# Kernel tuning notes

Hardware: AMD Instinct MI355X
Metric: run time of the kernel (lower is better)

Reference implementation:

```python
import jax, jax.numpy as jnp
import numpy as np

EPS = 1e-09

def setup_inputs() -> dict:
    key = jax.random.key(0)
    k1, k2, k3 = jax.random.split(key, 3)
    B, C, H, W = 16, 512, 64, 64
    K = 64  # node_num
    x = jax.random.normal(k1, (B, C, H, W), dtype=jnp.float32)
    anchor = jax.random.uniform(k2, (K, C), dtype=jnp.float32)
    sigma_raw = jax.random.uniform(k3, (K, C), dtype=jnp.float32)
    return {"x": x, "anchor": anchor, "sigma_raw": sigma_raw}

def _l2norm(v, axis):
    return v / jnp.maximum(jnp.linalg.norm(v, axis=axis, keepdims=True), 1e-12)

def reference(x, anchor, sigma_raw):
    B, C, H, W = x.shape
    K = anchor.shape[0]
    N = H * W
    sigma = jax.nn.sigmoid(sigma_raw)               # [K, C]
    xf = x.reshape(B, C, N).transpose(0, 2, 1)      # [B, N, C] descriptors

    # squared Mahalanobis-like distance ||(x - a_k)/s_k||^2 via expansion
    # (avoids materializing the [B, N, K, C] residual the torch loop builds)
    inv_s2 = 1.0 / (sigma * sigma)                  # [K, C]
    a_s2 = anchor * inv_s2                          # [K, C]
    const = jnp.sum(anchor * a_s2, axis=1)          # [K]
    d2 = (jnp.einsum('bnc,kc->bnk', xf * xf, inv_s2)
          - 2.0 * jnp.einsum('bnc,kc->bnk', xf, a_s2)
          + const[None, None, :])                   # [B, N, K]
    logits = (-0.5 * d2).transpose(0, 2, 1)         # [B, K, N]
    soft_assign = jax.nn.softmax(logits, axis=1)    # softmax over nodes

    # aggregation: nodes[b,k,c] = sum_n w * (x - a_k)/s_k / (sum_n w + eps)
    w_sum = jnp.sum(soft_assign, axis=2)            # [B, K]
    wx = jnp.einsum('bkn,bnc->bkc', soft_assign, xf)  # [B, K, C]
    nodes = (wx - w_sum[:, :, None] * anchor[None]) / sigma[None]
    nodes = nodes / (w_sum[:, :, None] + EPS)       # [B, K, C]

    nodes = _l2norm(nodes, axis=2)                  # intra-normalize per node
    flat = _l2norm(nodes.reshape(B, -1), axis=1)    # global L2
    # faithful to torch: flat [B, K*C] reinterpreted (no transpose) as [B, C, K]
    return flat.reshape(B, C, K), soft_assign
```

## Files before the change

kernel.cpp:

```cpp
#include <hip/hip_runtime.h>
#include <math.h>

#define B_ 16
#define C_ 512
#define N_ 4096
#define K_ 64

#define OFF_PBIG    0
#define OFF_CONST   131072
#define OFF_INVSIG  131136
#define OFF_WSUM    163904
#define OFF_GSUM    164928
#define OFF_WXP     165120

typedef short bf16x8 __attribute__((ext_vector_type(8)));
typedef float f32x16 __attribute__((ext_vector_type(16)));

union U4 { uint4 u; bf16x8 b; };

__device__ __forceinline__ unsigned hi16(float f) { return __float_as_uint(f) >> 16; }
__device__ __forceinline__ float fromhi(unsigned h) { return __uint_as_float(h << 16); }
__device__ __forceinline__ unsigned pk(float lo, float hi) {
  return (__float_as_uint(lo) >> 16) | (__float_as_uint(hi) & 0xFFFF0000u);
}

__global__ void k_prep(const float* __restrict__ anchor,
                       const float* __restrict__ sraw,
                       unsigned* __restrict__ pbig,
                       float* __restrict__ constk,
                       float* __restrict__ invsig,
                       float* __restrict__ wsum,
                       float* __restrict__ gsum) {
  const int k = blockIdx.x;
  const int t = threadIdx.x;
  __shared__ float s_is2[C_], s_m[C_];
  __shared__ float red[4];
  float part = 0.f;
#pragma unroll
  for (int r = 0; r < 2; r++) {
    int c = r * 256 + t;
    float a = anchor[k * C_ + c];
    float sg = 1.f / (1.f + __expf(-sraw[k * C_ + c]));
    float is = 1.f / sg;
    float is2 = is * is;
    s_is2[c] = is2;
    s_m[c] = -2.f * a * is2;
    invsig[k * C_ + c] = is;
    part = fmaf(a * a, is2, part);
  }
  float v = part;
#pragma unroll
  for (int off = 32; off; off >>= 1) v += __shfl_down(v, off);
  if ((t & 63) == 0) red[t >> 6] = v;
  __syncthreads();
  if (t == 0) constk[k] = red[0] + red[1] + red[2] + red[3];
#pragma unroll
  for (int r = 0; r < 2; r++) {
    int c = r * 256 + t;
    float is2 = s_is2[c], m = s_m[c];
    unsigned ih = hi16(is2);
    unsigned il = hi16(is2 - fromhi(ih));
    unsigned mh = hi16(m);
    unsigned ml = hi16(m - fromhi(mh));
    unsigned* p = pbig + (size_t)k * 2048 + c * 4;
    p[0] = ih | (il << 16);
    p[1] = ih | (mh << 16);
    p[2] = ml | (mh << 16);
    p[3] = 0u;
  }
  if (k == 0) {
    for (int i = t; i < B_ * K_; i += 256) wsum[i] = 0.f;
    if (t < B_) gsum[t] = 0.f;
  }
}

__global__ __launch_bounds__(256) void k_dist(
    const float* __restrict__ x,
    const unsigned* __restrict__ pbig,
    const float* __restrict__ constk,
    float* __restrict__ soft,
    float* __restrict__ wsum) {
  const int b = blockIdx.y;
  const int tid = threadIdx.x;
  const int wid = tid >> 6, lane = tid & 63, l31 = lane & 31, lh = lane >> 5;
  const int n0 = blockIdx.x * 128 + wid * 32;
  __shared__ unsigned ldsA[64 * 132];
  __shared__ float csh[64];
  if (tid < 64) csh[tid] = constk[tid];

  f32x16 acc[2];
#pragma unroll
  for (int kt = 0; kt < 2; kt++)
#pragma unroll
    for (int i = 0; i < 16; i++) acc[kt][i] = 0.f;

  const float* xb = x + (size_t)b * (C_ * N_);
  const uint4* src = (const uint4*)pbig;

  uint4 preg[8];
#pragma unroll
  for (int it = 0; it < 8; it++) {
    int flat = tid + it * 256;
    preg[it] = src[(size_t)(flat >> 5) * 512 + (flat & 31)];
  }
  float xcur[16], xnext[16];
#pragma unroll
  for (int i = 0; i < 16; i++)
    xcur[i] = xb[(size_t)(i * 2 + lh) * N_ + n0 + l31];

  for (int chunk = 0; chunk < 16; chunk++) {
#pragma unroll
    for (int it = 0; it < 8; it++) {
      int flat = tid + it * 256;
      *(uint4*)&ldsA[(flat >> 5) * 132 + (flat & 31) * 4] = preg[it];
    }
    __syncthreads();
    if (chunk < 15) {
#pragma unroll
      for (int it = 0; it < 8; it++) {
        int flat = tid + it * 256;
        preg[it] = src[(size_t)(flat >> 5) * 512 + (chunk + 1) * 32 + (flat & 31)];
      }
#pragma unroll
      for (int i = 0; i < 16; i++)
        xnext[i] = xb[(size_t)((chunk + 1) * 32 + i * 2 + lh) * N_ + n0 + l31];
    }
#pragma unroll
    for (int kstep = 0; kstep < 16; kstep++) {
      U4 a0, a1;
      a0.u = *(const uint4*)&ldsA[l31 * 132 + kstep * 8 + lh * 4];
      a1.u = *(const uint4*)&ldsA[(32 + l31) * 132 + kstep * 8 + lh * 4];
      float xv = xcur[kstep];
      float x2 = xv * xv;
      unsigned u = __float_as_uint(xv);
      unsigned u2 = __float_as_uint(x2);
      unsigned uhf = u & 0xFFFF0000u;
      unsigned u2hf = u2 & 0xFFFF0000u;
      float xl = xv - __uint_as_float(uhf);
      float x2l = x2 - __uint_as_float(u2hf);
      U4 bf;
      bf.u.x = (u2 >> 16) | u2hf;
      bf.u.y = (__float_as_uint(x2l) >> 16) | uhf;
      bf.u.z = (u >> 16) | (__float_as_uint(xl) & 0xFFFF0000u);
      bf.u.w = 0u;
      acc[0] = __builtin_amdgcn_mfma_f32_32x32x16_bf16(a0.b, bf.b, acc[0], 0, 0, 0);
      acc[1] = __builtin_amdgcn_mfma_f32_32x32x16_bf16(a1.b, bf.b, acc[1], 0, 0, 0);
    }
    __syncthreads();
#pragma unroll
    for (int i = 0; i < 16; i++) xcur[i] = xnext[i];
  }

  float mm = -3.4e38f;
#pragma unroll
  for (int kt = 0; kt < 2; kt++)
#pragma unroll
    for (int r = 0; r < 16; r++) {
      int k = kt * 32 + (r & 3) + 8 * (r >> 2) + 4 * lh;
      float l = -0.5f * (acc[kt][r] + csh[k]);
      acc[kt][r] = l;
      mm = fmaxf(mm, l);
    }
  mm = fmaxf(mm, __shfl_xor(mm, 32));
  float ss = 0.f;
#pragma unroll
  for (int kt = 0; kt < 2; kt++)
#pragma unroll
    for (int r = 0; r < 16; r++) {
      float e = __expf(acc[kt][r] - mm);
      acc[kt][r] = e;
      ss += e;
    }
  ss += __shfl_xor(ss, 32);
  float inv = 1.f / ss;

  float* softb = soft + (size_t)b * (K_ * N_);
#pragma unroll
  for (int kt = 0; kt < 2; kt++)
#pragma unroll
    for (int r = 0; r < 16; r++) {
      float w = acc[kt][r] * inv;
      acc[kt][r] = w;
      int k = kt * 32 + (r & 3) + 8 * (r >> 2) + 4 * lh;
      softb[(size_t)k * N_ + n0 + l31] = w;
    }
#pragma unroll
  for (int kt = 0; kt < 2; kt++)
#pragma unroll
    for (int r = 0; r < 16; r++) {
      float v = acc[kt][r];
      v += __shfl_xor(v, 1);
      v += __shfl_xor(v, 2);
      v += __shfl_xor(v, 4);
      v += __shfl_xor(v, 8);
      v += __shfl_xor(v, 16);
      if (l31 == 0) {
        int k = kt * 32 + (r & 3) + 8 * (r >> 2) + 4 * lh;
        atomicAdd(&wsum[b * K_ + k], v);
      }
    }
}

__global__ __launch_bounds__(256) void k_agg(const float* __restrict__ x,
                                             const float* __restrict__ soft,
                                             float* __restrict__ wxp) {
  const int ct = blockIdx.x;
  const int nt = blockIdx.y;
  const int b = blockIdx.z;
  const int tid = threadIdx.x;
  const int wid = tid >> 6, lane = tid & 63, l31 = lane & 31, lh = lane >> 5;
  __shared__ unsigned sA[64 * 36];
  __shared__ unsigned sX[128 * 36];

  f32x16 acc[2];
#pragma unroll
  for (int kt = 0; kt < 2; kt++)
#pragma unroll
    for (int i = 0; i < 16; i++) acc[kt][i] = 0.f;

  const float* sb = soft + (size_t)b * (K_ * N_) + nt * 1024;
  const float* xg = x + ((size_t)b * C_ + ct * 128) * N_ + nt * 1024;
  const int srow = tid >> 2, scol = (tid & 3) * 16;
  const int xrow = tid >> 1, xcol = (tid & 1) * 32;

  float4 sreg[4], xreg[8];
#pragma unroll
  for (int q = 0; q < 4; q++)
    sreg[q] = *(const float4*)&sb[(size_t)srow * N_ + scol + q * 4];
#pragma unroll
  for (int q = 0; q < 8; q++)
    xreg[q] = *(const float4*)&xg[(size_t)xrow * N_ + xcol + q * 4];

  for (int ch = 0; ch < 16; ch++) {
    {
      uint4 w0 = make_uint4(pk(sreg[0].x, sreg[0].y), pk(sreg[0].z, sreg[0].w),
                            pk(sreg[1].x, sreg[1].y), pk(sreg[1].z, sreg[1].w));
      uint4 w1 = make_uint4(pk(sreg[2].x, sreg[2].y), pk(sreg[2].z, sreg[2].w),
                            pk(sreg[3].x, sreg[3].y), pk(sreg[3].z, sreg[3].w));
      *(uint4*)&sA[srow * 36 + (tid & 3) * 8] = w0;
      *(uint4*)&sA[srow * 36 + (tid & 3) * 8 + 4] = w1;
#pragma unroll
      for (int h = 0; h < 4; h++) {
        uint4 v = make_uint4(
            pk(xreg[h * 2].x, xreg[h * 2].y), pk(xreg[h * 2].z, xreg[h * 2].w),
            pk(xreg[h * 2 + 1].x, xreg[h * 2 + 1].y),
            pk(xreg[h * 2 + 1].z, xreg[h * 2 + 1].w));
        *(uint4*)&sX[xrow * 36 + (tid & 1) * 16 + h * 4] = v;
      }
    }
    __syncthreads();
    if (ch < 15) {
      int base = (ch + 1) * 64;
#pragma unroll
      for (int q = 0; q < 4; q++)
        sreg[q] = *(const float4*)&sb[(size_t)srow * N_ + base + scol + q * 4];
#pragma unroll
      for (int q = 0; q < 8; q++)
        xreg[q] = *(const float4*)&xg[(size_t)xrow * N_ + base + xcol + q * 4];
    }
#pragma unroll
    for (int kk = 0; kk < 4; kk++) {
      U4 a0, a1, bf;
      a0.u = *(const uint4*)&sA[l31 * 36 + kk * 8 + lh * 4];
      a1.u = *(const uint4*)&sA[(32 + l31) * 36 + kk * 8 + lh * 4];
      bf.u = *(const uint4*)&sX[(wid * 32 + l31) * 36 + kk * 8 + lh * 4];
      acc[0] = __builtin_amdgcn_mfma_f32_32x32x16_bf16(a0.b, bf.b, acc[0], 0, 0, 0);
      acc[1] = __builtin_amdgcn_mfma_f32_32x32x16_bf16(a1.b, bf.b, acc[1], 0, 0, 0);
    }
    __syncthreads();
  }
  float* outp = wxp + (((size_t)nt * B_ + b) * K_) * C_ + ct * 128 + wid * 32 + l31;
#pragma unroll
  for (int kt = 0; kt < 2; kt++)
#pragma unroll
    for (int r = 0; r < 16; r++) {
      int k = kt * 32 + (r & 3) + 8 * (r >> 2) + 4 * lh;
      outp[(size_t)k * C_] = acc[kt][r];
    }
}

__global__ void k_nodes(const float* __restrict__ wxp,
                        const float* __restrict__ wsum,
                        const float* __restrict__ anchor,
                        const float* __restrict__ invsig,
                        float* __restrict__ out0,
                        float* __restrict__ gsum) {
  const int k = blockIdx.x, b = blockIdx.y;
  const int tid = threadIdx.x;
  float wsv = wsum[b * K_ + k];
  float winv = 1.f / (wsv + 1e-9f);
  float vals[4];
  float local = 0.f;
#pragma unroll
  for (int r = 0; r < 4; r++) {
    int c = r * 128 + tid;
    float w = 0.f;
#pragma unroll
    for (int p = 0; p < 4; p++)
      w += wxp[(((size_t)p * B_ + b) * K_ + k) * C_ + c];
    float v = (w - wsv * anchor[k * C_ + c]) * invsig[k * C_ + c] * winv;
    vals[r] = v;
    local = fmaf(v, v, local);
  }
  float v = local;
#pragma unroll
  for (int off = 32; off; off >>= 1) v += __shfl_down(v, off);
  __shared__ float red[2];
  if ((tid & 63) == 0) red[tid >> 6] = v;
  __syncthreads();
  float sumsq = red[0] + red[1];
  float norm = sqrtf(sumsq);
  float scale = 1.f / fmaxf(norm, 1e-12f);
#pragma unroll
  for (int r = 0; r < 4; r++) {
    int c = r * 128 + tid;
    out0[((size_t)b * K_ + k) * C_ + c] = vals[r] * scale;
  }
  if (tid == 0) atomicAdd(&gsum[b], sumsq * scale * scale);
}

__global__ void k_final(float* __restrict__ out0,
                        const float* __restrict__ gsum) {
  for (int i = blockIdx.x * 256 + threadIdx.x; i < B_ * K_ * C_;
       i += gridDim.x * 256) {
    int b = i >> 15;
    out0[i] = out0[i] * (1.f / fmaxf(sqrtf(gsum[b]), 1e-12f));
  }
}

extern "C" void kernel_launch(void* const* d_in, const int* in_sizes, int n_in,
                              void* d_out, int out_size, void* d_ws, size_t ws_size,
                              hipStream_t stream) {
  const float* x = (const float*)d_in[0];
  const float* anchor = (const float*)d_in[1];
  const float* sraw = (const float*)d_in[2];
  float* out0 = (float*)d_out;
  float* soft = out0 + (size_t)B_ * C_ * K_;
  float* ws = (float*)d_ws;

  unsigned* pbig = (unsigned*)(ws + OFF_PBIG);
  float* constk = ws + OFF_CONST;
  float* invsig = ws + OFF_INVSIG;
  float* wsum = ws + OFF_WSUM;
  float* gsum = ws + OFF_GSUM;
  float* wxp = ws + OFF_WXP;

  k_prep<<<K_, 256, 0, stream>>>(anchor, sraw, pbig, constk, invsig, wsum, gsum);
  k_dist<<<dim3(N_ / 128, B_), 256, 0, stream>>>(x, pbig, constk, soft, wsum);
  k_agg<<<dim3(C_ / 128, 4, B_), 256, 0, stream>>>(x, soft, wxp);
  k_nodes<<<dim3(K_, B_), 128, 0, stream>>>(wxp, wsum, anchor, invsig, out0,
                                            gsum);
  k_final<<<512, 256, 0, stream>>>(out0, gsum);
}
```

Measured before the change: 362.0 us.

## Stage x via direct global-to-LDS loads in k_dist and split k_agg finer with bf16 partials

```diff
diff --git a/kernel.cpp b/kernel.cpp
--- a/kernel.cpp
+++ b/kernel.cpp
@@ -23,6 +23,20 @@
 __device__ __forceinline__ unsigned pk(float lo, float hi) {
   return (__float_as_uint(lo) >> 16) | (__float_as_uint(hi) & 0xFFFF0000u);
 }
+__device__ __forceinline__ unsigned short bf16r(float f) {
+  unsigned u = __float_as_uint(f);
+  u += 0x7FFFu + ((u >> 16) & 1u);
+  return (unsigned short)(u >> 16);
+}
+
+#if defined(__has_builtin) && __has_builtin(__builtin_amdgcn_global_load_lds)
+#define GLD4(g, l)                                              \
+  __builtin_amdgcn_global_load_lds(                             \
+      (const __attribute__((address_space(1))) void*)(g),       \
+      (__attribute__((address_space(3))) void*)(l), 4, 0, 0)
+#else
+#define GLD4(g, l) (*(l) = *(g))
+#endif
 
 __global__ void k_prep(const float* __restrict__ anchor,
                        const float* __restrict__ sraw,
@@ -81,10 +95,13 @@
     float* __restrict__ soft,
     float* __restrict__ wsum) {
   const int b = blockIdx.y;
+  const int nblk = blockIdx.x * 128;
   const int tid = threadIdx.x;
   const int wid = tid >> 6, lane = tid & 63, l31 = lane & 31, lh = lane >> 5;
-  const int n0 = blockIdx.x * 128 + wid * 32;
-  __shared__ unsigned ldsA[64 * 132];
+  const int nw = nblk + wid * 32;
+
+  __shared__ unsigned ldsA[64 * 68];
+  __shared__ float ldsX[2][16 * 128];
   __shared__ float csh[64];
   if (tid < 64) csh[tid] = constk[tid];
 
@@ -97,40 +114,47 @@
   const float* xb = x + (size_t)b * (C_ * N_);
   const uint4* src = (const uint4*)pbig;
 
-  uint4 preg[8];
+  uint4 preg[4];
 #pragma unroll
   for (int it = 0; it < 8; it++) {
-    int flat = tid + it * 256;
-    preg[it] = src[(size_t)(flat >> 5) * 512 + (flat & 31)];
-  }
-  float xcur[16], xnext[16];
-#pragma unroll
-  for (int i = 0; i < 16; i++)
-    xcur[i] = xb[(size_t)(i * 2 + lh) * N_ + n0 + l31];
-
-  for (int chunk = 0; chunk < 16; chunk++) {
-#pragma unroll
-    for (int it = 0; it < 8; it++) {
-      int flat = tid + it * 256;
-      *(uint4*)&ldsA[(flat >> 5) * 132 + (flat & 31) * 4] = preg[it];
-    }
+    int f = it * 256 + tid;
+    GLD4(xb + (size_t)(f >> 7) * N_ + nblk + (f & 127), &ldsX[0][f]);
+  }
+#pragma unroll
+  for (int it = 0; it < 4; it++) {
+    int f = it * 256 + tid;
+    preg[it] = src[(size_t)(f >> 4) * 512 + (f & 15)];
+  }
+
+  for (int chunk = 0; chunk < 32; chunk++) {
     __syncthreads();
-    if (chunk < 15) {
+#pragma unroll
+    for (int it = 0; it < 4; it++) {
+      int f = it * 256 + tid;
+      *(uint4*)&ldsA[(f >> 4) * 68 + (f & 15) * 4] = preg[it];
+    }
+    __syncthreads();
+    if (chunk < 31) {
+      const int nc = chunk + 1;
 #pragma unroll
       for (int it = 0; it < 8; it++) {
-        int flat = tid + it * 256;
-        preg[it] = src[(size_t)(flat >> 5) * 512 + (chunk + 1) * 32 + (flat & 31)];
+        int f = it * 256 + tid;
+        GLD4(xb + (size_t)(nc * 16 + (f >> 7)) * N_ + nblk + (f & 127),
+             &ldsX[nc & 1][f]);
       }
 #pragma unroll
-      for (int i = 0; i < 16; i++)
-        xnext[i] = xb[(size_t)((chunk + 1) * 32 + i * 2 + lh) * N_ + n0 + l31];
-    }
-#pragma unroll
-    for (int kstep = 0; kstep < 16; kstep++) {
+      for (int it = 0; it < 4; it++) {
+        int f = it * 256 + tid;
+        preg[it] = src[(size_t)(f >> 4) * 512 + nc * 16 + (f & 15)];
+      }
+    }
+    const float* xc = &ldsX[chunk & 1][0];
+#pragma unroll
+    for (int kstep = 0; kstep < 8; kstep++) {
       U4 a0, a1;
-      a0.u = *(const uint4*)&ldsA[l31 * 132 + kstep * 8 + lh * 4];
-      a1.u = *(const uint4*)&ldsA[(32 + l31) * 132 + kstep * 8 + lh * 4];
-      float xv = xcur[kstep];
+      a0.u = *(const uint4*)&ldsA[l31 * 68 + kstep * 8 + lh * 4];
+      a1.u = *(const uint4*)&ldsA[(32 + l31) * 68 + kstep * 8 + lh * 4];
+      float xv = xc[(kstep * 2 + lh) * 128 + wid * 32 + l31];
       float x2 = xv * xv;
       unsigned u = __float_as_uint(xv);
       unsigned u2 = __float_as_uint(x2);
@@ -146,9 +170,6 @@
       acc[0] = __builtin_amdgcn_mfma_f32_32x32x16_bf16(a0.b, bf.b, acc[0], 0, 0, 0);
       acc[1] = __builtin_amdgcn_mfma_f32_32x32x16_bf16(a1.b, bf.b, acc[1], 0, 0, 0);
     }
-    __syncthreads();
-#pragma unroll
-    for (int i = 0; i < 16; i++) xcur[i] = xnext[i];
   }
 
   float mm = -3.4e38f;
@@ -182,7 +203,7 @@
       float w = acc[kt][r] * inv;
       acc[kt][r] = w;
       int k = kt * 32 + (r & 3) + 8 * (r >> 2) + 4 * lh;
-      softb[(size_t)k * N_ + n0 + l31] = w;
+      softb[(size_t)k * N_ + nw + l31] = w;
     }
 #pragma unroll
   for (int kt = 0; kt < 2; kt++)
@@ -203,10 +224,8 @@
 
 __global__ __launch_bounds__(256) void k_agg(const float* __restrict__ x,
                                              const float* __restrict__ soft,
-                                             float* __restrict__ wxp) {
-  const int ct = blockIdx.x;
-  const int nt = blockIdx.y;
-  const int b = blockIdx.z;
+                                             unsigned short* __restrict__ wxp) {
+  const int ct = blockIdx.x, nt = blockIdx.y, b = blockIdx.z;
   const int tid = threadIdx.x;
   const int wid = tid >> 6, lane = tid & 63, l31 = lane & 31, lh = lane >> 5;
   __shared__ unsigned sA[64 * 36];
@@ -218,45 +237,38 @@
 #pragma unroll
     for (int i = 0; i < 16; i++) acc[kt][i] = 0.f;
 
-  const float* sb = soft + (size_t)b * (K_ * N_) + nt * 1024;
-  const float* xg = x + ((size_t)b * C_ + ct * 128) * N_ + nt * 1024;
-  const int srow = tid >> 2, scol = (tid & 3) * 16;
-  const int xrow = tid >> 1, xcol = (tid & 1) * 32;
+  const float* sb = soft + (size_t)b * (K_ * N_) + nt * 512;
+  const float* xg = x + ((size_t)b * C_ + ct * 128) * N_ + nt * 512;
+  const int row16 = tid >> 4, col4 = tid & 15;
 
   float4 sreg[4], xreg[8];
 #pragma unroll
-  for (int q = 0; q < 4; q++)
-    sreg[q] = *(const float4*)&sb[(size_t)srow * N_ + scol + q * 4];
+  for (int p = 0; p < 4; p++)
+    sreg[p] = *(const float4*)&sb[(size_t)(p * 16 + row16) * N_ + col4 * 4];
 #pragma unroll
   for (int q = 0; q < 8; q++)
-    xreg[q] = *(const float4*)&xg[(size_t)xrow * N_ + xcol + q * 4];
-
-  for (int ch = 0; ch < 16; ch++) {
-    {
-      uint4 w0 = make_uint4(pk(sreg[0].x, sreg[0].y), pk(sreg[0].z, sreg[0].w),
-                            pk(sreg[1].x, sreg[1].y), pk(sreg[1].z, sreg[1].w));
-      uint4 w1 = make_uint4(pk(sreg[2].x, sreg[2].y), pk(sreg[2].z, sreg[2].w),
-                            pk(sreg[3].x, sreg[3].y), pk(sreg[3].z, sreg[3].w));
-      *(uint4*)&sA[srow * 36 + (tid & 3) * 8] = w0;
-      *(uint4*)&sA[srow * 36 + (tid & 3) * 8 + 4] = w1;
-#pragma unroll
-      for (int h = 0; h < 4; h++) {
-        uint4 v = make_uint4(
-            pk(xreg[h * 2].x, xreg[h * 2].y), pk(xreg[h * 2].z, xreg[h * 2].w),
-            pk(xreg[h * 2 + 1].x, xreg[h * 2 + 1].y),
-            pk(xreg[h * 2 + 1].z, xreg[h * 2 + 1].w));
-        *(uint4*)&sX[xrow * 36 + (tid & 1) * 16 + h * 4] = v;
-      }
+    xreg[q] = *(const float4*)&xg[(size_t)(q * 16 + row16) * N_ + col4 * 4];
+
+  for (int ch = 0; ch < 8; ch++) {
+#pragma unroll
+    for (int p = 0; p < 4; p++) {
+      uint2 v = make_uint2(pk(sreg[p].x, sreg[p].y), pk(sreg[p].z, sreg[p].w));
+      *(uint2*)&sA[(p * 16 + row16) * 36 + col4 * 2] = v;
+    }
+#pragma unroll
+    for (int q = 0; q < 8; q++) {
+      uint2 v = make_uint2(pk(xreg[q].x, xreg[q].y), pk(xreg[q].z, xreg[q].w));
+      *(uint2*)&sX[(q * 16 + row16) * 36 + col4 * 2] = v;
     }
     __syncthreads();
-    if (ch < 15) {
-      int base = (ch + 1) * 64;
-#pragma unroll
-      for (int q = 0; q < 4; q++)
-        sreg[q] = *(const float4*)&sb[(size_t)srow * N_ + base + scol + q * 4];
+    if (ch < 7) {
+      const int nb = (ch + 1) * 64;
+#pragma unroll
+      for (int p = 0; p < 4; p++)
+        sreg[p] = *(const float4*)&sb[(size_t)(p * 16 + row16) * N_ + nb + col4 * 4];
 #pragma unroll
       for (int q = 0; q < 8; q++)
-        xreg[q] = *(const float4*)&xg[(size_t)xrow * N_ + base + xcol + q * 4];
+        xreg[q] = *(const float4*)&xg[(size_t)(q * 16 + row16) * N_ + nb + col4 * 4];
     }
 #pragma unroll
     for (int kk = 0; kk < 4; kk++) {
@@ -269,17 +281,18 @@
     }
     __syncthreads();
   }
-  float* outp = wxp + (((size_t)nt * B_ + b) * K_) * C_ + ct * 128 + wid * 32 + l31;
+  unsigned short* outp =
+      wxp + ((size_t)(nt * B_ + b) * K_) * C_ + ct * 128 + wid * 32 + l31;
 #pragma unroll
   for (int kt = 0; kt < 2; kt++)
 #pragma unroll
     for (int r = 0; r < 16; r++) {
       int k = kt * 32 + (r & 3) + 8 * (r >> 2) + 4 * lh;
-      outp[(size_t)k * C_] = acc[kt][r];
-    }
-}
-
-__global__ void k_nodes(const float* __restrict__ wxp,
+      outp[(size_t)k * C_] = bf16r(acc[kt][r]);
+    }
+}
+
+__global__ void k_nodes(const unsigned short* __restrict__ wxp,
                         const float* __restrict__ wsum,
                         const float* __restrict__ anchor,
                         const float* __restrict__ invsig,
@@ -296,8 +309,8 @@
     int c = r * 128 + tid;
     float w = 0.f;
 #pragma unroll
-    for (int p = 0; p < 4; p++)
-      w += wxp[(((size_t)p * B_ + b) * K_ + k) * C_ + c];
+    for (int p = 0; p < 8; p++)
+      w += fromhi(wxp[(((size_t)p * B_ + b) * K_ + k) * C_ + c]);
     float v = (w - wsv * anchor[k * C_ + c]) * invsig[k * C_ + c] * winv;
     vals[r] = v;
     local = fmaf(v, v, local);
@@ -343,11 +356,11 @@
   float* invsig = ws + OFF_INVSIG;
   float* wsum = ws + OFF_WSUM;
   float* gsum = ws + OFF_GSUM;
-  float* wxp = ws + OFF_WXP;
+  unsigned short* wxp = (unsigned short*)(ws + OFF_WXP);
 
   k_prep<<<K_, 256, 0, stream>>>(anchor, sraw, pbig, constk, invsig, wsum, gsum);
   k_dist<<<dim3(N_ / 128, B_), 256, 0, stream>>>(x, pbig, constk, soft, wsum);
-  k_agg<<<dim3(C_ / 128, 4, B_), 256, 0, stream>>>(x, soft, wxp);
+  k_agg<<<dim3(C_ / 128, 8, B_), 256, 0, stream>>>(x, soft, wxp);
   k_nodes<<<dim3(K_, B_), 128, 0, stream>>>(wxp, wsum, anchor, invsig, out0,
                                             gsum);
   k_final<<<512, 256, 0, stream>>>(out0, gsum);
```

Measured after the change: 347.5 us. 4.0% less time.
